# Optimization experiments

Hardware: AMD Instinct MI355X
Metric: run time of the kernel (lower is better)

## Reference

```python
import jax, jax.numpy as jnp
import numpy as np

B, S, D, H = 4, 2048, 1024, 16
HD = D // H

def setup_inputs() -> dict:
    key = jax.random.key(0)
    ks = jax.random.split(key, 11)
    s = 1.0 / np.sqrt(D)
    def lin(k):
        kw, kb = jax.random.split(k)
        return (jax.random.uniform(kw, (D, D), jnp.float32, -s, s),
                jax.random.uniform(kb, (D,), jnp.float32, -s, s))
    Wq, bq = lin(ks[0]); Wk, bk = lin(ks[1]); Wv, bv = lin(ks[2]); Wo, bo = lin(ks[3])
    return {
        "query": jax.random.normal(ks[4], (B, S, D), jnp.float32),
        "key": jax.random.normal(ks[5], (B, S, D), jnp.float32),
        "value": jax.random.normal(ks[6], (B, S, D), jnp.float32),
        "Wq": Wq, "bq": bq, "Wk": Wk, "bk": bk,
        "Wv": Wv, "bv": bv, "Wo": Wo, "bo": bo,
    }

def reference(query, key, value, Wq, bq, Wk, bk, Wv, bv, Wo, bo):
    def split_heads(x):  # [B,S,D] -> [B,H,S,HD]
        return x.reshape(B, S, H, HD).transpose(0, 2, 1, 3)
    q = split_heads(query @ Wq + bq)
    k = split_heads(key @ Wk + bk)
    v = split_heads(value @ Wv + bv)
    scores = jnp.einsum('bhqd,bhkd->bhqk', q, k) / np.sqrt(HD)
    probs = jax.nn.softmax(scores, axis=-1)
    ctx = jnp.einsum('bhqk,bhkd->bhqd', probs, v)
    ctx = ctx.transpose(0, 2, 1, 3).reshape(B, S, D)
    return ctx @ Wo + bo
```

## Files before the change

### kernel.cpp

```cpp
#include <hip/hip_runtime.h>
#include <hip/hip_bf16.h>

#define B_ 4
#define S_ 2048
#define D_ 1024
#define H_ 16
#define HD_ 64
#define M_ (B_*S_)

typedef __bf16 bf16;
typedef bf16 bf16x8 __attribute__((ext_vector_type(8)));
typedef bf16 bf16x4 __attribute__((ext_vector_type(4)));
typedef float f32x4 __attribute__((ext_vector_type(4)));

__device__ __forceinline__ void gload_lds16(const void* g, void* l) {
  __builtin_amdgcn_global_load_lds((const __attribute__((address_space(1))) void*)g,
                                   (__attribute__((address_space(3))) void*)l, 16, 0, 0);
}

__global__ __launch_bounds__(256)
void wtrans_kernel(const float* __restrict__ Wq, const float* __restrict__ Wk,
                   const float* __restrict__ Wv, const float* __restrict__ Wo,
                   bf16* __restrict__ Wqt, bf16* __restrict__ Wkt,
                   bf16* __restrict__ Wvt, bf16* __restrict__ Wot) {
  __shared__ float tile[64][65];
  const float* W; bf16* Wt;
  switch (blockIdx.z) {
    case 0: W = Wq; Wt = Wqt; break;
    case 1: W = Wk; Wt = Wkt; break;
    case 2: W = Wv; Wt = Wvt; break;
    default: W = Wo; Wt = Wot; break;
  }
  int n0 = blockIdx.x * 64, k0 = blockIdx.y * 64;
  int tx = threadIdx.x & 63, ty = threadIdx.x >> 6;
#pragma unroll
  for (int i = 0; i < 16; i++) {
    int k = ty + i * 4;
    tile[k][tx] = W[(size_t)(k0 + k) * D_ + n0 + tx];
  }
  __syncthreads();
#pragma unroll
  for (int i = 0; i < 16; i++) {
    int n = ty + i * 4;
    Wt[(size_t)(n0 + n) * D_ + k0 + tx] = (bf16)tile[tx][n];
  }
}

#define QSCALE 0.18033688011112042f

__global__ __launch_bounds__(256)
void proj_gemm_kernel(const float* __restrict__ Aq, const float* __restrict__ Ak,
                      const float* __restrict__ Av,
                      const bf16* __restrict__ Wqt, const bf16* __restrict__ Wkt,
                      const bf16* __restrict__ Wvt,
                      const float* __restrict__ bq, const float* __restrict__ bk,
                      const float* __restrict__ bv,
                      bf16* __restrict__ qb, bf16* __restrict__ kb, bf16* __restrict__ vbT) {
  __shared__ float Asf[128 * 64];
  __shared__ bf16  Bs[128 * 64];
  const float* A; const bf16* Bt; const float* bias;
  if (blockIdx.z == 0)      { A = Aq; Bt = Wqt; bias = bq; }
  else if (blockIdx.z == 1) { A = Ak; Bt = Wkt; bias = bk; }
  else                      { A = Av; Bt = Wvt; bias = bv; }

  const int orig = blockIdx.y * gridDim.x + blockIdx.x;
  const int swz  = (orig & 7) * 64 + (orig >> 3);
  const int n0 = (swz & 7) * 128, m0 = (swz >> 3) * 128;

  const int tid = threadIdx.x;
  const int lane = tid & 63, w = tid >> 6;
  const int wr = w >> 1, wc = w & 1;
  const int l15 = lane & 15, quad = lane >> 4;
  const int arow_sub = lane >> 4, achk = lane & 15;
  const int brow_sub = lane >> 3, bchk = lane & 7;

  f32x4 acc[4][4] = {};

  for (int kt = 0; kt < D_ / 64; kt++) {
    const int k0 = kt * 64;
#pragma unroll
    for (int t = 0; t < 8; t++) {
      int r0 = w * 32 + t * 4;
      int row = r0 + arow_sub;
      int cg = achk ^ (row & 15);
      gload_lds16(A + (size_t)(m0 + row) * D_ + k0 + cg * 4, &Asf[r0 * 64]);
    }
#pragma unroll
    for (int t = 0; t < 4; t++) {
      int r0 = w * 32 + t * 8;
      int row = r0 + brow_sub;
      int cg = bchk ^ (row & 7);
      gload_lds16(Bt + (size_t)(n0 + row) * D_ + k0 + cg * 8, &Bs[r0 * 64]);
    }
    __syncthreads();

#pragma unroll
    for (int ks = 0; ks < 2; ks++) {
      bf16x8 a[4], b[4];
#pragma unroll
      for (int fm = 0; fm < 4; fm++) {
        int row = wr * 64 + fm * 16 + l15;
        int cl = (ks * 8 + quad * 2) ^ (row & 15);
        f32x4 lo = *(const f32x4*)(&Asf[row * 64 + cl * 4]);
        f32x4 hi = *(const f32x4*)(&Asf[row * 64 + (cl ^ 1) * 4]);
        bf16x8 av;
        av[0] = (bf16)lo[0]; av[1] = (bf16)lo[1]; av[2] = (bf16)lo[2]; av[3] = (bf16)lo[3];
        av[4] = (bf16)hi[0]; av[5] = (bf16)hi[1]; av[6] = (bf16)hi[2]; av[7] = (bf16)hi[3];
        a[fm] = av;
      }
#pragma unroll
      for (int fn = 0; fn < 4; fn++) {
        int row = wc * 64 + fn * 16 + l15;
        b[fn] = *(const bf16x8*)(&Bs[row * 64 + (((ks * 4 + quad) ^ (row & 7)) * 8)]);
      }
#pragma unroll
      for (int fm = 0; fm < 4; fm++)
#pragma unroll
        for (int fn = 0; fn < 4; fn++)
          acc[fm][fn] = __builtin_amdgcn_mfma_f32_16x16x32_bf16(a[fm], b[fn], acc[fm][fn], 0, 0, 0);
    }
    __syncthreads();
  }

  if (blockIdx.z < 2) {
    bf16* C = (blockIdx.z == 0) ? qb : kb;
    float scale = (blockIdx.z == 0) ? QSCALE : 1.0f;
#pragma unroll
    for (int fm = 0; fm < 4; fm++) {
      int row = m0 + wr * 64 + fm * 16 + quad * 4;
#pragma unroll
      for (int fn = 0; fn < 4; fn++) {
        int col = n0 + wc * 64 + fn * 16 + l15;
        float bval = bias[col];
#pragma unroll
        for (int r = 0; r < 4; r++)
          C[(size_t)(row + r) * D_ + col] = (bf16)((acc[fm][fn][r] + bval) * scale);
      }
    }
  } else {
#pragma unroll
    for (int fm = 0; fm < 4; fm++) {
      int row = m0 + wr * 64 + fm * 16 + quad * 4;
#pragma unroll
      for (int fn = 0; fn < 4; fn++) {
        int col = n0 + wc * 64 + fn * 16 + l15;
        float bval = bias[col];
        bf16x4 pk;
#pragma unroll
        for (int r = 0; r < 4; r++) pk[r] = (bf16)(acc[fm][fn][r] + bval);
        *(bf16x4*)(vbT + (size_t)col * M_ + row) = pk;
      }
    }
  }
}

#define LPS 72

__global__ __launch_bounds__(256)
void attn_kernel(const bf16* __restrict__ qb, const bf16* __restrict__ kb,
                 const bf16* __restrict__ vbT, bf16* __restrict__ ctxb) {
  __shared__ bf16 Ks[2][64 * 64];
  __shared__ bf16 Vs[2][64 * 64];
  __shared__ bf16 Ps[128 * LPS];
  __shared__ float Lf[128];

  const int orig = blockIdx.y * gridDim.x + blockIdx.x;
  const int swz  = (orig & 7) * 128 + (orig >> 3);
  const int bh = swz >> 4;
  const int b = bh >> 4, h = bh & 15;
  const int q0 = (swz & 15) * 128;

  const int tid = threadIdx.x, lane = tid & 63, w = tid >> 6;
  const int l15 = lane & 15, quad = lane >> 4;

  const size_t baseQ = ((size_t)(b * S_ + q0)) * D_ + h * HD_;

  bf16x8 qf[2][2];
#pragma unroll
  for (int fm = 0; fm < 2; fm++)
#pragma unroll
    for (int ks = 0; ks < 2; ks++)
      qf[fm][ks] = *(const bf16x8*)(qb + baseQ + (size_t)(w * 32 + fm * 16 + l15) * D_ + ks * 32 + quad * 8);

  f32x4 o[2][4] = {};
  float li[2] = {0.f, 0.f};

  const int srow_i = lane >> 3;
  const int schunk = lane & 7;

  auto stage = [&](int buf, int kt) {
#pragma unroll
    for (int t = 0; t < 2; t++) {
      const int r0 = w * 16 + t * 8;
      const int row = r0 + srow_i;
      const int c = schunk ^ (row & 7);
      const bf16* gK = kb + ((size_t)(b * S_ + kt * 64 + row)) * D_ + h * 64 + c * 8;
      gload_lds16(gK, &Ks[buf][r0 * 64]);
      const bf16* gV = vbT + ((size_t)(h * 64 + row)) * M_ + b * S_ + kt * 64 + c * 8;
      gload_lds16(gV, &Vs[buf][r0 * 64]);
    }
  };

  stage(0, 0);
  __syncthreads();

  for (int kt = 0; kt < S_ / 64; kt++) {
    const int buf = kt & 1;
    if (kt + 1 < S_ / 64) stage(buf ^ 1, kt + 1);

    f32x4 st[4][2] = {};
#pragma unroll
    for (int ks = 0; ks < 2; ks++) {
#pragma unroll
      for (int fk = 0; fk < 4; fk++) {
        const int key = fk * 16 + l15;
        bf16x8 kf = *(const bf16x8*)(&Ks[buf][key * 64 + (((ks * 4 + quad) ^ (key & 7)) * 8)]);
#pragma unroll
        for (int fq = 0; fq < 2; fq++)
          st[fk][fq] = __builtin_amdgcn_mfma_f32_16x16x32_bf16(kf, qf[fq][ks], st[fk][fq], 0, 0, 0);
      }
    }

#pragma unroll
    for (int fq = 0; fq < 2; fq++) {
      const int prow = (w * 32 + fq * 16 + l15) * LPS;
#pragma unroll
      for (int fk = 0; fk < 4; fk++) {
        float p0 = __builtin_amdgcn_exp2f(st[fk][fq][0]);
        float p1 = __builtin_amdgcn_exp2f(st[fk][fq][1]);
        float p2 = __builtin_amdgcn_exp2f(st[fk][fq][2]);
        float p3 = __builtin_amdgcn_exp2f(st[fk][fq][3]);
        li[fq] += (p0 + p1) + (p2 + p3);
        bf16x4 pk;
        pk[0] = (bf16)p0; pk[1] = (bf16)p1; pk[2] = (bf16)p2; pk[3] = (bf16)p3;
        *(bf16x4*)(&Ps[prow + fk * 16 + quad * 4]) = pk;
      }
    }

#pragma unroll
    for (int ks2 = 0; ks2 < 2; ks2++) {
      bf16x8 pf[2], vf[4];
#pragma unroll
      for (int fm = 0; fm < 2; fm++)
        pf[fm] = *(const bf16x8*)(&Ps[(w * 32 + fm * 16 + l15) * LPS + ks2 * 32 + quad * 8]);
#pragma unroll
      for (int fd = 0; fd < 4; fd++) {
        const int d = fd * 16 + l15;
        vf[fd] = *(const bf16x8*)(&Vs[buf][d * 64 + (((ks2 * 4 + quad) ^ (d & 7)) * 8)]);
      }
#pragma unroll
      for (int fm = 0; fm < 2; fm++)
#pragma unroll
        for (int fd = 0; fd < 4; fd++)
          o[fm][fd] = __builtin_amdgcn_mfma_f32_16x16x32_bf16(pf[fm], vf[fd], o[fm][fd], 0, 0, 0);
    }
    __syncthreads();
  }

#pragma unroll
  for (int fq = 0; fq < 2; fq++) {
    float l = li[fq];
    l += __shfl_xor(l, 16);
    l += __shfl_xor(l, 32);
    if (quad == 0) Lf[w * 32 + fq * 16 + l15] = l;
  }
#pragma unroll
  for (int fm = 0; fm < 2; fm++) {
    f32x4 l4 = *(const f32x4*)(&Lf[w * 32 + fm * 16 + quad * 4]);
#pragma unroll
    for (int r = 0; r < 4; r++) {
      float inv = 1.0f / l4[r];
      int row = w * 32 + fm * 16 + quad * 4 + r;
#pragma unroll
      for (int fd = 0; fd < 4; fd++)
        ctxb[baseQ + (size_t)row * D_ + fd * 16 + l15] = (bf16)(o[fm][fd][r] * inv);
    }
  }
}

__global__ __launch_bounds__(256)
void out_gemm_kernel(const bf16* __restrict__ A, const bf16* __restrict__ Bt,
                     const float* __restrict__ bias, float* __restrict__ Cout) {
  __shared__ bf16 As[128 * 64];
  __shared__ bf16 Bs[128 * 64];
  const int orig = blockIdx.y * gridDim.x + blockIdx.x;
  const int swz  = (orig & 7) * 64 + (orig >> 3);
  const int n0 = (swz & 7) * 128, m0 = (swz >> 3) * 128;

  const int tid = threadIdx.x;
  const int lane = tid & 63, w = tid >> 6;
  const int wr = w >> 1, wc = w & 1;
  const int l15 = lane & 15, quad = lane >> 4;
  const int srow = lane >> 3, schunk = lane & 7;

  f32x4 acc[4][4] = {};

  for (int kt = 0; kt < D_ / 64; kt++) {
    const int k0 = kt * 64;
#pragma unroll
    for (int t = 0; t < 4; t++) {
      int r0 = w * 32 + t * 8;
      int row = r0 + srow;
      int cg = schunk ^ (row & 7);
      gload_lds16(A + (size_t)(m0 + row) * D_ + k0 + cg * 8, &As[r0 * 64]);
      gload_lds16(Bt + (size_t)(n0 + row) * D_ + k0 + cg * 8, &Bs[r0 * 64]);
    }
    __syncthreads();

#pragma unroll
    for (int ks = 0; ks < 2; ks++) {
      bf16x8 a[4], b[4];
#pragma unroll
      for (int fm = 0; fm < 4; fm++) {
        int row = wr * 64 + fm * 16 + l15;
        a[fm] = *(const bf16x8*)(&As[row * 64 + (((ks * 4 + quad) ^ (row & 7)) * 8)]);
      }
#pragma unroll
      for (int fn = 0; fn < 4; fn++) {
        int row = wc * 64 + fn * 16 + l15;
        b[fn] = *(const bf16x8*)(&Bs[row * 64 + (((ks * 4 + quad) ^ (row & 7)) * 8)]);
      }
#pragma unroll
      for (int fm = 0; fm < 4; fm++)
#pragma unroll
        for (int fn = 0; fn < 4; fn++)
          acc[fm][fn] = __builtin_amdgcn_mfma_f32_16x16x32_bf16(a[fm], b[fn], acc[fm][fn], 0, 0, 0);
    }
    __syncthreads();
  }
#pragma unroll
  for (int fm = 0; fm < 4; fm++) {
    int row = m0 + wr * 64 + fm * 16 + quad * 4;
#pragma unroll
    for (int fn = 0; fn < 4; fn++) {
      int col = n0 + wc * 64 + fn * 16 + l15;
      float bval = bias[col];
#pragma unroll
      for (int r = 0; r < 4; r++)
        Cout[(size_t)(row + r) * D_ + col] = acc[fm][fn][r] + bval;
    }
  }
}

extern "C" void kernel_launch(void* const* d_in, const int* in_sizes, int n_in,
                              void* d_out, int out_size, void* d_ws, size_t ws_size,
                              hipStream_t stream) {
  const float* query = (const float*)d_in[0];
  const float* key   = (const float*)d_in[1];
  const float* value = (const float*)d_in[2];
  const float* Wq = (const float*)d_in[3];
  const float* bq = (const float*)d_in[4];
  const float* Wk = (const float*)d_in[5];
  const float* bk = (const float*)d_in[6];
  const float* Wv = (const float*)d_in[7];
  const float* bv = (const float*)d_in[8];
  const float* Wo = (const float*)d_in[9];
  const float* bo = (const float*)d_in[10];
  float* out = (float*)d_out;

  char* ws = (char*)d_ws;
  const size_t WT_BYTES = (size_t)D_ * D_ * sizeof(bf16);
  const size_t MD_BYTES = (size_t)M_ * D_ * sizeof(bf16);
  bf16* Wqt  = (bf16*)(ws);
  bf16* Wkt  = (bf16*)(ws + WT_BYTES);
  bf16* Wvt  = (bf16*)(ws + 2 * WT_BYTES);
  bf16* Wot  = (bf16*)(ws + 3 * WT_BYTES);
  bf16* qb   = (bf16*)(ws + 4 * WT_BYTES);
  bf16* kb   = (bf16*)(ws + 4 * WT_BYTES + MD_BYTES);
  bf16* vbT  = (bf16*)(ws + 4 * WT_BYTES + 2 * MD_BYTES);
  bf16* ctxb = (bf16*)(ws + 4 * WT_BYTES + 3 * MD_BYTES);

  wtrans_kernel<<<dim3(D_ / 64, D_ / 64, 4), 256, 0, stream>>>(
      Wq, Wk, Wv, Wo, Wqt, Wkt, Wvt, Wot);

  proj_gemm_kernel<<<dim3(D_ / 128, M_ / 128, 3), 256, 0, stream>>>(
      query, key, value, Wqt, Wkt, Wvt, bq, bk, bv, qb, kb, vbT);

  attn_kernel<<<dim3(S_ / 128, B_ * H_), 256, 0, stream>>>(qb, kb, vbT, ctxb);

  out_gemm_kernel<<<dim3(D_ / 128, M_ / 128), 256, 0, stream>>>(ctxb, Wot, bo, out);
}
```

Measured before the change: 367.1 us.

## Double-buffer projection and output GEMMs, convert A to bf16 via registers, prioritise MFMA

The projection GEMM now loads fp32 activations into registers for the next K tile, converts them to bf16 and writes them into a double-buffered bf16 LDS tile after the current tile's MFMAs. This replaces the fp32 LDS staging and the per-fragment conversion at read time. The output GEMM gets a double-buffered LDS pipeline that issues the next tile's async loads before computing the current one. The attention kernel wraps its MFMA blocks in s_setprio to favour matrix issue across waves. The cost is twice the LDS per block, which may lower occupancy, plus extra register pressure from the prefetched A values.

```diff
diff --git a/kernel.cpp b/kernel.cpp
--- a/kernel.cpp
+++ b/kernel.cpp
@@ -56,8 +56,8 @@
                       const float* __restrict__ bq, const float* __restrict__ bk,
                       const float* __restrict__ bv,
                       bf16* __restrict__ qb, bf16* __restrict__ kb, bf16* __restrict__ vbT) {
-  __shared__ float Asf[128 * 64];
-  __shared__ bf16  Bs[128 * 64];
+  __shared__ bf16 As[2][128 * 64];
+  __shared__ bf16 Bs[2][128 * 64];
   const float* A; const bf16* Bt; const float* bias;
   if (blockIdx.z == 0)      { A = Aq; Bt = Wqt; bias = bq; }
   else if (blockIdx.z == 1) { A = Ak; Bt = Wkt; bias = bk; }
@@ -71,53 +71,79 @@
   const int lane = tid & 63, w = tid >> 6;
   const int wr = w >> 1, wc = w & 1;
   const int l15 = lane & 15, quad = lane >> 4;
-  const int arow_sub = lane >> 4, achk = lane & 15;
-  const int brow_sub = lane >> 3, bchk = lane & 7;
+  const int arow4 = lane >> 4, c4 = lane & 15;
+  const int brow = lane >> 3, bchk = lane & 7;
 
   f32x4 acc[4][4] = {};
+  f32x4 ar[8];
+
+#pragma unroll
+  for (int t = 0; t < 8; t++) {
+    int row = w * 32 + t * 4 + arow4;
+    ar[t] = *(const f32x4*)(A + (size_t)(m0 + row) * D_ + c4 * 4);
+  }
+#pragma unroll
+  for (int t = 0; t < 4; t++) {
+    int r0 = w * 32 + t * 8;
+    int row = r0 + brow;
+    int cg = bchk ^ (row & 7);
+    gload_lds16(Bt + (size_t)(n0 + row) * D_ + cg * 8, &Bs[0][r0 * 64]);
+  }
+#pragma unroll
+  for (int t = 0; t < 8; t++) {
+    int row = w * 32 + t * 4 + arow4;
+    bf16x4 pk;
+    pk[0] = (bf16)ar[t][0]; pk[1] = (bf16)ar[t][1];
+    pk[2] = (bf16)ar[t][2]; pk[3] = (bf16)ar[t][3];
+    *(bf16x4*)(&As[0][row * 64 + (((c4 >> 1) ^ (row & 7)) * 8 + (c4 & 1) * 4)]) = pk;
+  }
+  __syncthreads();
 
   for (int kt = 0; kt < D_ / 64; kt++) {
-    const int k0 = kt * 64;
-#pragma unroll
-    for (int t = 0; t < 8; t++) {
-      int r0 = w * 32 + t * 4;
-      int row = r0 + arow_sub;
-      int cg = achk ^ (row & 15);
-      gload_lds16(A + (size_t)(m0 + row) * D_ + k0 + cg * 4, &Asf[r0 * 64]);
-    }
-#pragma unroll
-    for (int t = 0; t < 4; t++) {
-      int r0 = w * 32 + t * 8;
-      int row = r0 + brow_sub;
-      int cg = bchk ^ (row & 7);
-      gload_lds16(Bt + (size_t)(n0 + row) * D_ + k0 + cg * 8, &Bs[r0 * 64]);
-    }
-    __syncthreads();
-
+    const int cur = kt & 1, nxt = cur ^ 1;
+    if (kt + 1 < D_ / 64) {
+      const int k0 = (kt + 1) * 64;
+#pragma unroll
+      for (int t = 0; t < 8; t++) {
+        int row = w * 32 + t * 4 + arow4;
+        ar[t] = *(const f32x4*)(A + (size_t)(m0 + row) * D_ + k0 + c4 * 4);
+      }
+#pragma unroll
+      for (int t = 0; t < 4; t++) {
+        int r0 = w * 32 + t * 8;
+        int row = r0 + brow;
+        int cg = bchk ^ (row & 7);
+        gload_lds16(Bt + (size_t)(n0 + row) * D_ + k0 + cg * 8, &Bs[nxt][r0 * 64]);
+      }
+    }
 #pragma unroll
     for (int ks = 0; ks < 2; ks++) {
       bf16x8 a[4], b[4];
 #pragma unroll
       for (int fm = 0; fm < 4; fm++) {
         int row = wr * 64 + fm * 16 + l15;
-        int cl = (ks * 8 + quad * 2) ^ (row & 15);
-        f32x4 lo = *(const f32x4*)(&Asf[row * 64 + cl * 4]);
-        f32x4 hi = *(const f32x4*)(&Asf[row * 64 + (cl ^ 1) * 4]);
-        bf16x8 av;
-        av[0] = (bf16)lo[0]; av[1] = (bf16)lo[1]; av[2] = (bf16)lo[2]; av[3] = (bf16)lo[3];
-        av[4] = (bf16)hi[0]; av[5] = (bf16)hi[1]; av[6] = (bf16)hi[2]; av[7] = (bf16)hi[3];
-        a[fm] = av;
+        a[fm] = *(const bf16x8*)(&As[cur][row * 64 + (((ks * 4 + quad) ^ (row & 7)) * 8)]);
       }
 #pragma unroll
       for (int fn = 0; fn < 4; fn++) {
         int row = wc * 64 + fn * 16 + l15;
-        b[fn] = *(const bf16x8*)(&Bs[row * 64 + (((ks * 4 + quad) ^ (row & 7)) * 8)]);
+        b[fn] = *(const bf16x8*)(&Bs[cur][row * 64 + (((ks * 4 + quad) ^ (row & 7)) * 8)]);
       }
 #pragma unroll
       for (int fm = 0; fm < 4; fm++)
 #pragma unroll
         for (int fn = 0; fn < 4; fn++)
           acc[fm][fn] = __builtin_amdgcn_mfma_f32_16x16x32_bf16(a[fm], b[fn], acc[fm][fn], 0, 0, 0);
+    }
+    if (kt + 1 < D_ / 64) {
+#pragma unroll
+      for (int t = 0; t < 8; t++) {
+        int row = w * 32 + t * 4 + arow4;
+        bf16x4 pk;
+        pk[0] = (bf16)ar[t][0]; pk[1] = (bf16)ar[t][1];
+        pk[2] = (bf16)ar[t][2]; pk[3] = (bf16)ar[t][3];
+        *(bf16x4*)(&As[nxt][row * 64 + (((c4 >> 1) ^ (row & 7)) * 8 + (c4 & 1) * 4)]) = pk;
+      }
     }
     __syncthreads();
   }
@@ -209,6 +235,7 @@
     if (kt + 1 < S_ / 64) stage(buf ^ 1, kt + 1);
 
     f32x4 st[4][2] = {};
+    __builtin_amdgcn_s_setprio(1);
 #pragma unroll
     for (int ks = 0; ks < 2; ks++) {
 #pragma unroll
@@ -220,6 +247,7 @@
           st[fk][fq] = __builtin_amdgcn_mfma_f32_16x16x32_bf16(kf, qf[fq][ks], st[fk][fq], 0, 0, 0);
       }
     }
+    __builtin_amdgcn_s_setprio(0);
 
 #pragma unroll
     for (int fq = 0; fq < 2; fq++) {
@@ -248,11 +276,13 @@
         const int d = fd * 16 + l15;
         vf[fd] = *(const bf16x8*)(&Vs[buf][d * 64 + (((ks2 * 4 + quad) ^ (d & 7)) * 8)]);
       }
+      __builtin_amdgcn_s_setprio(1);
 #pragma unroll
       for (int fm = 0; fm < 2; fm++)
 #pragma unroll
         for (int fd = 0; fd < 4; fd++)
           o[fm][fd] = __builtin_amdgcn_mfma_f32_16x16x32_bf16(pf[fm], vf[fd], o[fm][fd], 0, 0, 0);
+      __builtin_amdgcn_s_setprio(0);
     }
     __syncthreads();
   }
@@ -281,8 +311,8 @@
 __global__ __launch_bounds__(256)
 void out_gemm_kernel(const bf16* __restrict__ A, const bf16* __restrict__ Bt,
                      const float* __restrict__ bias, float* __restrict__ Cout) {
-  __shared__ bf16 As[128 * 64];
-  __shared__ bf16 Bs[128 * 64];
+  __shared__ bf16 As[2][128 * 64];
+  __shared__ bf16 Bs[2][128 * 64];
   const int orig = blockIdx.y * gridDim.x + blockIdx.x;
   const int swz  = (orig & 7) * 64 + (orig >> 3);
   const int n0 = (swz & 7) * 128, m0 = (swz >> 3) * 128;
@@ -295,17 +325,24 @@
 
   f32x4 acc[4][4] = {};
 
-  for (int kt = 0; kt < D_ / 64; kt++) {
+  auto stage = [&](int buf, int kt) {
     const int k0 = kt * 64;
 #pragma unroll
     for (int t = 0; t < 4; t++) {
       int r0 = w * 32 + t * 8;
       int row = r0 + srow;
       int cg = schunk ^ (row & 7);
-      gload_lds16(A + (size_t)(m0 + row) * D_ + k0 + cg * 8, &As[r0 * 64]);
-      gload_lds16(Bt + (size_t)(n0 + row) * D_ + k0 + cg * 8, &Bs[r0 * 64]);
-    }
-    __syncthreads();
+      gload_lds16(A + (size_t)(m0 + row) * D_ + k0 + cg * 8, &As[buf][r0 * 64]);
+      gload_lds16(Bt + (size_t)(n0 + row) * D_ + k0 + cg * 8, &Bs[buf][r0 * 64]);
+    }
+  };
+
+  stage(0, 0);
+  __syncthreads();
+
+  for (int kt = 0; kt < D_ / 64; kt++) {
+    const int cur = kt & 1;
+    if (kt + 1 < D_ / 64) stage(cur ^ 1, kt + 1);
 
 #pragma unroll
     for (int ks = 0; ks < 2; ks++) {
@@ -313,12 +350,12 @@
 #pragma unroll
       for (int fm = 0; fm < 4; fm++) {
         int row = wr * 64 + fm * 16 + l15;
-        a[fm] = *(const bf16x8*)(&As[row * 64 + (((ks * 4 + quad) ^ (row & 7)) * 8)]);
+        a[fm] = *(const bf16x8*)(&As[cur][row * 64 + (((ks * 4 + quad) ^ (row & 7)) * 8)]);
       }
 #pragma unroll
       for (int fn = 0; fn < 4; fn++) {
         int row = wc * 64 + fn * 16 + l15;
-        b[fn] = *(const bf16x8*)(&Bs[row * 64 + (((ks * 4 + quad) ^ (row & 7)) * 8)]);
+        b[fn] = *(const bf16x8*)(&Bs[cur][row * 64 + (((ks * 4 + quad) ^ (row & 7)) * 8)]);
       }
 #pragma unroll
       for (int fm = 0; fm < 4; fm++)
```

Result: slower. 399.9 us (+9.0%).

## Pre-convert QKV inputs to bf16 and raise wave priority around attention MFMAs

Applied to the files above, without the earlier changes.

Adds a separate kernel that converts the fp32 query/key/value activations to bf16 before the projection GEMM. The GEMM can then stage bf16 A tiles directly with the same swizzle as B, which halves LDS use and drops the per-fragment fp32-to-bf16 conversion from the inner loop. The cost is an extra launch and an extra pass over memory: it reads 96MB of fp32 and writes 48MB of bf16, and the GEMM then re-reads the bf16 copy. The attention kernel also wraps its MFMA blocks in s_setprio so waves issuing matrix ops are scheduled ahead of others.

```diff
diff --git a/kernel.cpp b/kernel.cpp
--- a/kernel.cpp
+++ b/kernel.cpp
@@ -46,22 +46,41 @@
   }
 }
 
+__global__ __launch_bounds__(256)
+void qkv_cvt_kernel(const float* __restrict__ q, const float* __restrict__ k,
+                    const float* __restrict__ v,
+                    bf16* __restrict__ qo, bf16* __restrict__ ko, bf16* __restrict__ vo) {
+  const float* src; bf16* dst;
+  switch (blockIdx.y) {
+    case 0: src = q; dst = qo; break;
+    case 1: src = k; dst = ko; break;
+    default: src = v; dst = vo; break;
+  }
+  size_t i = ((size_t)blockIdx.x * 256 + threadIdx.x) * 8;
+  f32x4 a = *(const f32x4*)(src + i);
+  f32x4 b = *(const f32x4*)(src + i + 4);
+  bf16x8 o;
+  o[0] = (bf16)a[0]; o[1] = (bf16)a[1]; o[2] = (bf16)a[2]; o[3] = (bf16)a[3];
+  o[4] = (bf16)b[0]; o[5] = (bf16)b[1]; o[6] = (bf16)b[2]; o[7] = (bf16)b[3];
+  *(bf16x8*)(dst + i) = o;
+}
+
 #define QSCALE 0.18033688011112042f
 
 __global__ __launch_bounds__(256)
-void proj_gemm_kernel(const float* __restrict__ Aq, const float* __restrict__ Ak,
-                      const float* __restrict__ Av,
+void proj_gemm_kernel(const bf16* __restrict__ Aqb, const bf16* __restrict__ Akb,
+                      const bf16* __restrict__ Avb,
                       const bf16* __restrict__ Wqt, const bf16* __restrict__ Wkt,
                       const bf16* __restrict__ Wvt,
                       const float* __restrict__ bq, const float* __restrict__ bk,
                       const float* __restrict__ bv,
                       bf16* __restrict__ qb, bf16* __restrict__ kb, bf16* __restrict__ vbT) {
-  __shared__ float Asf[128 * 64];
-  __shared__ bf16  Bs[128 * 64];
-  const float* A; const bf16* Bt; const float* bias;
-  if (blockIdx.z == 0)      { A = Aq; Bt = Wqt; bias = bq; }
-  else if (blockIdx.z == 1) { A = Ak; Bt = Wkt; bias = bk; }
-  else                      { A = Av; Bt = Wvt; bias = bv; }
+  __shared__ bf16 As[128 * 64];
+  __shared__ bf16 Bs[128 * 64];
+  const bf16* A; const bf16* Bt; const float* bias;
+  if (blockIdx.z == 0)      { A = Aqb; Bt = Wqt; bias = bq; }
+  else if (blockIdx.z == 1) { A = Akb; Bt = Wkt; bias = bk; }
+  else                      { A = Avb; Bt = Wvt; bias = bv; }
 
   const int orig = blockIdx.y * gridDim.x + blockIdx.x;
   const int swz  = (orig & 7) * 64 + (orig >> 3);
@@ -71,25 +90,18 @@
   const int lane = tid & 63, w = tid >> 6;
   const int wr = w >> 1, wc = w & 1;
   const int l15 = lane & 15, quad = lane >> 4;
-  const int arow_sub = lane >> 4, achk = lane & 15;
-  const int brow_sub = lane >> 3, bchk = lane & 7;
+  const int srow = lane >> 3, schunk = lane & 7;
 
   f32x4 acc[4][4] = {};
 
   for (int kt = 0; kt < D_ / 64; kt++) {
     const int k0 = kt * 64;
 #pragma unroll
-    for (int t = 0; t < 8; t++) {
-      int r0 = w * 32 + t * 4;
-      int row = r0 + arow_sub;
-      int cg = achk ^ (row & 15);
-      gload_lds16(A + (size_t)(m0 + row) * D_ + k0 + cg * 4, &Asf[r0 * 64]);
-    }
-#pragma unroll
     for (int t = 0; t < 4; t++) {
       int r0 = w * 32 + t * 8;
-      int row = r0 + brow_sub;
-      int cg = bchk ^ (row & 7);
+      int row = r0 + srow;
+      int cg = schunk ^ (row & 7);
+      gload_lds16(A + (size_t)(m0 + row) * D_ + k0 + cg * 8, &As[r0 * 64]);
       gload_lds16(Bt + (size_t)(n0 + row) * D_ + k0 + cg * 8, &Bs[r0 * 64]);
     }
     __syncthreads();
@@ -100,13 +112,7 @@
 #pragma unroll
       for (int fm = 0; fm < 4; fm++) {
         int row = wr * 64 + fm * 16 + l15;
-        int cl = (ks * 8 + quad * 2) ^ (row & 15);
-        f32x4 lo = *(const f32x4*)(&Asf[row * 64 + cl * 4]);
-        f32x4 hi = *(const f32x4*)(&Asf[row * 64 + (cl ^ 1) * 4]);
-        bf16x8 av;
-        av[0] = (bf16)lo[0]; av[1] = (bf16)lo[1]; av[2] = (bf16)lo[2]; av[3] = (bf16)lo[3];
-        av[4] = (bf16)hi[0]; av[5] = (bf16)hi[1]; av[6] = (bf16)hi[2]; av[7] = (bf16)hi[3];
-        a[fm] = av;
+        a[fm] = *(const bf16x8*)(&As[row * 64 + (((ks * 4 + quad) ^ (row & 7)) * 8)]);
       }
 #pragma unroll
       for (int fn = 0; fn < 4; fn++) {
@@ -209,6 +215,7 @@
     if (kt + 1 < S_ / 64) stage(buf ^ 1, kt + 1);
 
     f32x4 st[4][2] = {};
+    __builtin_amdgcn_s_setprio(1);
 #pragma unroll
     for (int ks = 0; ks < 2; ks++) {
 #pragma unroll
@@ -220,6 +227,7 @@
           st[fk][fq] = __builtin_amdgcn_mfma_f32_16x16x32_bf16(kf, qf[fq][ks], st[fk][fq], 0, 0, 0);
       }
     }
+    __builtin_amdgcn_s_setprio(0);
 
 #pragma unroll
     for (int fq = 0; fq < 2; fq++) {
@@ -248,11 +256,13 @@
         const int d = fd * 16 + l15;
         vf[fd] = *(const bf16x8*)(&Vs[buf][d * 64 + (((ks2 * 4 + quad) ^ (d & 7)) * 8)]);
       }
+      __builtin_amdgcn_s_setprio(1);
 #pragma unroll
       for (int fm = 0; fm < 2; fm++)
 #pragma unroll
         for (int fd = 0; fd < 4; fd++)
           o[fm][fd] = __builtin_amdgcn_mfma_f32_16x16x32_bf16(pf[fm], vf[fd], o[fm][fd], 0, 0, 0);
+      __builtin_amdgcn_s_setprio(0);
     }
     __syncthreads();
   }
@@ -369,12 +379,18 @@
   bf16* kb   = (bf16*)(ws + 4 * WT_BYTES + MD_BYTES);
   bf16* vbT  = (bf16*)(ws + 4 * WT_BYTES + 2 * MD_BYTES);
   bf16* ctxb = (bf16*)(ws + 4 * WT_BYTES + 3 * MD_BYTES);
+  bf16* qcv  = ctxb;
+  bf16* kcv  = (bf16*)(ws + 4 * WT_BYTES + 4 * MD_BYTES);
+  bf16* vcv  = (bf16*)(ws + 4 * WT_BYTES + 5 * MD_BYTES);
 
   wtrans_kernel<<<dim3(D_ / 64, D_ / 64, 4), 256, 0, stream>>>(
       Wq, Wk, Wv, Wo, Wqt, Wkt, Wvt, Wot);
 
+  qkv_cvt_kernel<<<dim3((size_t)M_ * D_ / 2048, 3), 256, 0, stream>>>(
+      query, key, value, qcv, kcv, vcv);
+
   proj_gemm_kernel<<<dim3(D_ / 128, M_ / 128, 3), 256, 0, stream>>>(
-      query, key, value, Wqt, Wkt, Wvt, bq, bk, bv, qb, kb, vbT);
+      qcv, kcv, vcv, Wqt, Wkt, Wvt, bq, bk, bv, qb, kb, vbT);
 
   attn_kernel<<<dim3(S_ / 128, B_ * H_), 256, 0, stream>>>(qb, kb, vbT, ctxb);
 
```

New measurement: 359.6 us. 1.02x faster.
